# Kernel optimization log

Measured on AMD Instinct MI355X. Metric: run time of the kernel, lower is better.

The kernel has to match this reference:

```python
import jax, jax.numpy as jnp
import numpy as np

B, C, H, W = 16, 64, 128, 128
K = 3
Z = 128


def setup_inputs() -> dict:
    key = jax.random.key(0)
    k1, k2, k3, k4 = jax.random.split(key, 4)
    x = jax.random.normal(k1, (B, C, H, W), dtype=jnp.float32)
    z = jax.random.normal(k2, (B, Z), dtype=jnp.float32)
    # generator: Linear(Z -> C*C*K*K), scaled for stable conv outputs
    gen_w = jax.random.normal(k3, (Z, C * C * K * K), dtype=jnp.float32) * 0.02
    gen_b = jax.random.normal(k4, (C * C * K * K,), dtype=jnp.float32) * 0.02
    return {"x": x, "z": z, "gen_w": gen_w, "gen_b": gen_b}


def _conv_one(xi, wi):
    # xi: [C,H,W], wi: [C_out,C_in,K,K]; 'same' padding conv, no bias
    out = jax.lax.conv_general_dilated(
        xi[None], wi, window_strides=(1, 1), padding="SAME",
        dimension_numbers=("NCHW", "OIHW", "NCHW"))
    return out[0]


def reference(x, z, gen_w, gen_b):
    # per-sample weight generation: [B, C*C*K*K] -> [B, C, C, K, K]
    weight = (z @ gen_w + gen_b).reshape(B, C, C, K, K)
    # batched per-sample convolution (replaces the python loop over batch)
    return jax.vmap(_conv_one)(x, weight)
```

## Files before the change

kernel.cpp:

```cpp
#include <hip/hip_runtime.h>
#include <hip/hip_bf16.h>

typedef __attribute__((ext_vector_type(4))) float f32x4;
typedef __attribute__((ext_vector_type(8))) short short8;

#define B_ 16
#define C_ 64
#define H_ 128
#define W_ 128
#define Z_ 128
#define IDXN (C_*C_*9)
#define NT 18

__device__ __forceinline__ unsigned short f2bf(float f) {
  __hip_bfloat16 h = __float2bfloat16(f);
  return *reinterpret_cast<unsigned short*>(&h);
}

__global__ __launch_bounds__(256) void wgen_k(
    const float* __restrict__ z, const float* __restrict__ gw,
    const float* __restrict__ gb, unsigned short* __restrict__ wfrag) {
  __shared__ __align__(16) float zs[B_*Z_];
  int t = threadIdx.x;
#pragma unroll
  for (int i = 0; i < 8; ++i) zs[i*256 + t] = z[i*256 + t];
  __syncthreads();
  int lane = t & 63, bg = t >> 6;
  int b0 = bg*4;
  int idx0 = blockIdx.x*128 + lane;
  float acc[4][2];
  float bv0 = gb[idx0], bv1 = gb[idx0 + 64];
#pragma unroll
  for (int bi = 0; bi < 4; ++bi) { acc[bi][0] = bv0; acc[bi][1] = bv1; }

  for (int z0 = 0; z0 < Z_; z0 += 4) {
    float ga[4], gbv[4];
#pragma unroll
    for (int zi = 0; zi < 4; ++zi) {
      ga[zi]  = gw[(size_t)(z0+zi)*IDXN + idx0];
      gbv[zi] = gw[(size_t)(z0+zi)*IDXN + idx0 + 64];
    }
#pragma unroll
    for (int bi = 0; bi < 4; ++bi) {
      f32x4 zq = *reinterpret_cast<const f32x4*>(&zs[(b0+bi)*Z_ + z0]);
      acc[bi][0] = fmaf(zq[0], ga[0], fmaf(zq[1], ga[1], fmaf(zq[2], ga[2], fmaf(zq[3], ga[3], acc[bi][0]))));
      acc[bi][1] = fmaf(zq[0], gbv[0], fmaf(zq[1], gbv[1], fmaf(zq[2], gbv[2], fmaf(zq[3], gbv[3], acc[bi][1]))));
    }
  }
#pragma unroll
  for (int ni = 0; ni < 2; ++ni) {
    int idx = idx0 + ni*64;
    int kw = idx % 3, r1 = idx/3;
    int kh = r1 % 3, r2 = r1/3;
    int ci = r2 & 63, co = r2 >> 6;
    int k = (kh*3 + kw)*C_ + ci;
    int ts = k >> 5, kin = k & 31;
    int lm = (co & 15) | ((kin >> 3) << 4);
    int j = kin & 7, m = co >> 4;
    int base = ((ts*4 + m)*64 + lm)*8 + j;
#pragma unroll
    for (int bi = 0; bi < 4; ++bi)
      wfrag[(size_t)(b0+bi)*(NT*4*64*8) + base] = f2bf(acc[bi][ni]);
  }
}

__global__ __launch_bounds__(256) void conv_k(
    const float* __restrict__ x,
    const unsigned short* __restrict__ wfrag,
    float* __restrict__ out) {
  __shared__ __align__(16) unsigned char xs[4*130*128];
  int orig = blockIdx.x;
  int blk = (orig & 7)*128 + (orig >> 3);
  int b = blk >> 6;
  int h0 = (blk & 63)*2;
  int tid = threadIdx.x;
  int v = tid >> 6, lane = tid & 63;

  {
    int hh = h0 - 1 + v;
    bool hv = (hh >= 0) & (hh < H_);
    unsigned char* ldsrow = xs + v*(130*128);
    if (hv) {
      if (lane < 16) {
        int s = (lane < 8) ? lane : (1024 + lane - 8 + 8);
        uint4 zv; zv.x = 0; zv.y = 0; zv.z = 0; zv.w = 0;
        *reinterpret_cast<uint4*>(ldsrow + s*16) = zv;
      }
      const float* xrow = x + (((size_t)b*C_)*H_ + hh)*W_;
      int w0 = 2*lane, col0 = w0 + 1, col1 = w0 + 2;
      int g = lane >> 3;
#pragma unroll
      for (int c8 = 0; c8 < 8; ++c8) {
        int chunk = (c8 + g) & 7;
        float2 v2[8];
#pragma unroll
        for (int j = 0; j < 8; ++j)
          v2[j] = *reinterpret_cast<const float2*>(xrow + (size_t)(chunk*8 + j)*(H_*W_) + w0);
        uint4 o0, o1;
        unsigned short* s0 = reinterpret_cast<unsigned short*>(&o0);
        unsigned short* s1 = reinterpret_cast<unsigned short*>(&o1);
#pragma unroll
        for (int j = 0; j < 8; ++j) {
          s0[j] = f2bf(v2[j].x);
          s1[j] = f2bf(v2[j].y);
        }
        int a0 = col0*128 + (((chunk ^ col0) & 7) << 4);
        int a1 = col1*128 + (((chunk ^ col1) & 7) << 4);
        *reinterpret_cast<uint4*>(ldsrow + a0) = o0;
        *reinterpret_cast<uint4*>(ldsrow + a1) = o1;
      }
    } else {
      uint4 zv; zv.x = 0; zv.y = 0; zv.z = 0; zv.w = 0;
#pragma unroll
      for (int it = 0; it < 17; ++it) {
        int di = it*64 + lane;
        if (di < 1040) *reinterpret_cast<uint4*>(ldsrow + di*16) = zv;
      }
    }
  }
  __syncthreads();

  int l15 = lane & 15, lhi = lane >> 4;
  int phr = v >> 1, pw0 = (v & 1)*64;
  f32x4 acc[4][4];
#pragma unroll
  for (int mp = 0; mp < 4; ++mp)
#pragma unroll
    for (int nc = 0; nc < 4; ++nc)
      acc[mp][nc] = (f32x4){0.f, 0.f, 0.f, 0.f};

  const unsigned short* wb = wfrag + (size_t)b*(NT*4*64*8);
#pragma unroll
  for (int t = 0; t < NT; ++t) {
    int kk = t >> 1, kh = kk/3, kw = kk%3, half = t & 1;
    short8 wf[4];
#pragma unroll
    for (int nc = 0; nc < 4; ++nc)
      wf[nc] = *reinterpret_cast<const short8*>(wb + ((t*4 + nc)*64 + lane)*8);
    int chunk = half*4 + lhi;
    short8 xa[4];
#pragma unroll
    for (int mp = 0; mp < 4; ++mp) {
      int col = pw0 + mp*16 + l15 + kw;
      int addr = ((phr + kh)*130 + col)*128 + (((chunk ^ col) & 7) << 4);
      xa[mp] = *reinterpret_cast<const short8*>(&xs[addr]);
    }
#pragma unroll
    for (int mp = 0; mp < 4; ++mp)
#pragma unroll
      for (int nc = 0; nc < 4; ++nc)
        acc[mp][nc] = __builtin_amdgcn_mfma_f32_16x16x32_bf16(xa[mp], wf[nc], acc[mp][nc], 0, 0, 0);
  }

  int ph = h0 + phr;
#pragma unroll
  for (int nc = 0; nc < 4; ++nc) {
    int co = nc*16 + l15;
    float* op = out + (((size_t)b*C_ + co)*H_ + ph)*W_;
#pragma unroll
    for (int mp = 0; mp < 4; ++mp) {
      int pix = pw0 + mp*16 + lhi*4;
      *reinterpret_cast<f32x4*>(op + pix) = acc[mp][nc];
    }
  }
}

__global__ void sentinel_k(float* out, int n) {
  int i = blockIdx.x*256 + threadIdx.x;
  if (i < n) out[i] = 1.0e6f;
}

extern "C" void kernel_launch(void* const* d_in, const int* in_sizes, int n_in,
                              void* d_out, int out_size, void* d_ws, size_t ws_size,
                              hipStream_t stream) {
  const float* x  = (const float*)d_in[0];
  const float* z  = (const float*)d_in[1];
  const float* gw = (const float*)d_in[2];
  const float* gb = (const float*)d_in[3];
  float* out = (float*)d_out;

  size_t wfrag_elems = (size_t)B_*IDXN;
  size_t need = wfrag_elems*sizeof(unsigned short);
  if (ws_size < need) {
    sentinel_k<<<(out_size + 255)/256, 256, 0, stream>>>(out, out_size);
    return;
  }
  unsigned short* wfrag = (unsigned short*)d_ws;

  wgen_k <<<IDXN/128, 256, 0, stream>>>(z, gw, gb, wfrag);
  conv_k <<<B_*(H_/2),256, 0, stream>>>(x, wfrag, out);
}
```

Measured before the change: 50.45 us.

## Split conv block into 512 threads with halved per-wave output channels

Raises the conv kernel block from 256 to 512 threads, so each wave computes two output-channel tiles instead of four. This halves accumulator registers and raises occupancy. The input row staging is split across twice as many waves, each loading half the channel chunks. Weight fragments are now software-prefetched one tap ahead, and the first fragments are issued before the barrier to hide global latency. In exchange, each wave re-reads the same LDS input fragments for fewer MFMAs, which raises LDS traffic per unit of work.

Measured after the change: 51.23 us. Within noise of the previous version (+1.5%).

```diff
diff --git a/kernel.cpp b/kernel.cpp
--- a/kernel.cpp
+++ b/kernel.cpp
@@ -64,7 +64,7 @@
   }
 }
 
-__global__ __launch_bounds__(256) void conv_k(
+__global__ __launch_bounds__(512, 4) void conv_k(
     const float* __restrict__ x,
     const unsigned short* __restrict__ wfrag,
     float* __restrict__ out) {
@@ -77,12 +77,13 @@
   int v = tid >> 6, lane = tid & 63;
 
   {
-    int hh = h0 - 1 + v;
+    int r = v >> 1, hf = v & 1;
+    int hh = h0 - 1 + r;
     bool hv = (hh >= 0) & (hh < H_);
-    unsigned char* ldsrow = xs + v*(130*128);
+    unsigned char* ldsrow = xs + r*(130*128);
     if (hv) {
-      if (lane < 16) {
-        int s = (lane < 8) ? lane : (1024 + lane - 8 + 8);
+      if (lane < 8) {
+        int s = hf ? (1032 + lane) : lane;
         uint4 zv; zv.x = 0; zv.y = 0; zv.z = 0; zv.w = 0;
         *reinterpret_cast<uint4*>(ldsrow + s*16) = zv;
       }
@@ -90,8 +91,8 @@
       int w0 = 2*lane, col0 = w0 + 1, col1 = w0 + 2;
       int g = lane >> 3;
 #pragma unroll
-      for (int c8 = 0; c8 < 8; ++c8) {
-        int chunk = (c8 + g) & 7;
+      for (int i = 0; i < 4; ++i) {
+        int chunk = (hf*4 + i + g) & 7;
         float2 v2[8];
 #pragma unroll
         for (int j = 0; j < 8; ++j)
@@ -112,31 +113,38 @@
     } else {
       uint4 zv; zv.x = 0; zv.y = 0; zv.z = 0; zv.w = 0;
 #pragma unroll
-      for (int it = 0; it < 17; ++it) {
+      for (int it = 0; it < 9; ++it) {
         int di = it*64 + lane;
-        if (di < 1040) *reinterpret_cast<uint4*>(ldsrow + di*16) = zv;
+        if (di < 520) *reinterpret_cast<uint4*>(ldsrow + (hf*520 + di)*16) = zv;
       }
     }
   }
+
+  int l15 = lane & 15, lhi = lane >> 4;
+  int phr = v >> 2, pw0 = ((v >> 1) & 1)*64;
+  int mt0 = (v & 1)*2;
+  const unsigned short* wb = wfrag + (size_t)b*(NT*4*64*8);
+
+  short8 wf0 = *reinterpret_cast<const short8*>(wb + (((0*4 + mt0 + 0)*64 + lane)*8));
+  short8 wf1 = *reinterpret_cast<const short8*>(wb + (((0*4 + mt0 + 1)*64 + lane)*8));
+
   __syncthreads();
 
-  int l15 = lane & 15, lhi = lane >> 4;
-  int phr = v >> 1, pw0 = (v & 1)*64;
-  f32x4 acc[4][4];
+  f32x4 acc[4][2];
 #pragma unroll
   for (int mp = 0; mp < 4; ++mp)
 #pragma unroll
-    for (int nc = 0; nc < 4; ++nc)
+    for (int nc = 0; nc < 2; ++nc)
       acc[mp][nc] = (f32x4){0.f, 0.f, 0.f, 0.f};
 
-  const unsigned short* wb = wfrag + (size_t)b*(NT*4*64*8);
 #pragma unroll
   for (int t = 0; t < NT; ++t) {
     int kk = t >> 1, kh = kk/3, kw = kk%3, half = t & 1;
-    short8 wf[4];
-#pragma unroll
-    for (int nc = 0; nc < 4; ++nc)
-      wf[nc] = *reinterpret_cast<const short8*>(wb + ((t*4 + nc)*64 + lane)*8);
+    short8 nf0, nf1;
+    if (t + 1 < NT) {
+      nf0 = *reinterpret_cast<const short8*>(wb + ((((t+1)*4 + mt0 + 0)*64 + lane)*8));
+      nf1 = *reinterpret_cast<const short8*>(wb + ((((t+1)*4 + mt0 + 1)*64 + lane)*8));
+    }
     int chunk = half*4 + lhi;
     short8 xa[4];
 #pragma unroll
@@ -146,16 +154,17 @@
       xa[mp] = *reinterpret_cast<const short8*>(&xs[addr]);
     }
 #pragma unroll
-    for (int mp = 0; mp < 4; ++mp)
-#pragma unroll
-      for (int nc = 0; nc < 4; ++nc)
-        acc[mp][nc] = __builtin_amdgcn_mfma_f32_16x16x32_bf16(xa[mp], wf[nc], acc[mp][nc], 0, 0, 0);
+    for (int mp = 0; mp < 4; ++mp) {
+      acc[mp][0] = __builtin_amdgcn_mfma_f32_16x16x32_bf16(xa[mp], wf0, acc[mp][0], 0, 0, 0);
+      acc[mp][1] = __builtin_amdgcn_mfma_f32_16x16x32_bf16(xa[mp], wf1, acc[mp][1], 0, 0, 0);
+    }
+    wf0 = nf0; wf1 = nf1;
   }
 
   int ph = h0 + phr;
 #pragma unroll
-  for (int nc = 0; nc < 4; ++nc) {
-    int co = nc*16 + l15;
+  for (int nc = 0; nc < 2; ++nc) {
+    int co = (mt0 + nc)*16 + l15;
     float* op = out + (((size_t)b*C_ + co)*H_ + ph)*W_;
 #pragma unroll
     for (int mp = 0; mp < 4; ++mp) {
@@ -188,5 +197,5 @@
   unsigned short* wfrag = (unsigned short*)d_ws;
 
   wgen_k <<<IDXN/128, 256, 0, stream>>>(z, gw, gb, wfrag);
-  conv_k <<<B_*(H_/2),256, 0, stream>>>(x, wfrag, out);
-}
+  conv_k <<<B_*(H_/2), 512, 0, stream>>>(x, wfrag, out);
+}
```

## Enlarge conv tile to four output rows and double-buffer MFMA operand loads

Applied to the files above, without the earlier changes.

Each conv block now handles four output rows with 512 threads, staging six input rows into LDS instead of four rows for two outputs. This reduces redundant halo reads of x from global memory. The inner loop also prefetches the next tap's weight and LDS fragments while the current MFMAs run. In exchange, LDS use per block rises to about 100KB, which lowers resident blocks per CU, and two waves sit idle during staging.

After: 52.43 us. 1.04x slower.

```diff
diff --git a/kernel.cpp b/kernel.cpp
--- a/kernel.cpp
+++ b/kernel.cpp
@@ -9,6 +9,7 @@
 #define H_ 128
 #define W_ 128
 #define Z_ 128
+#define HW_ (H_*W_)
 #define IDXN (C_*C_*9)
 #define NT 18
 
@@ -64,46 +65,45 @@
   }
 }
 
-__global__ __launch_bounds__(256) void conv_k(
+__global__ __launch_bounds__(512, 2) void conv_k(
     const float* __restrict__ x,
     const unsigned short* __restrict__ wfrag,
     float* __restrict__ out) {
-  __shared__ __align__(16) unsigned char xs[4*130*128];
+  __shared__ __align__(16) unsigned char xs[6*130*128];
   int orig = blockIdx.x;
-  int blk = (orig & 7)*128 + (orig >> 3);
-  int b = blk >> 6;
-  int h0 = (blk & 63)*2;
+  int blk = (orig & 7)*64 + (orig >> 3);
+  int b = blk >> 5;
+  int h0 = (blk & 31)*4;
   int tid = threadIdx.x;
   int v = tid >> 6, lane = tid & 63;
 
-  {
+  if (tid < 96) {
+    int sl = tid >> 4, cc = (tid >> 3) & 1, ch = tid & 7;
+    int col = cc ? 129 : 0;
+    uint4 zv; zv.x = 0; zv.y = 0; zv.z = 0; zv.w = 0;
+    *reinterpret_cast<uint4*>(&xs[(sl*130 + col)*128 + ch*16]) = zv;
+  }
+
+  if (v < 6) {
     int hh = h0 - 1 + v;
     bool hv = (hh >= 0) & (hh < H_);
     unsigned char* ldsrow = xs + v*(130*128);
     if (hv) {
-      if (lane < 16) {
-        int s = (lane < 8) ? lane : (1024 + lane - 8 + 8);
-        uint4 zv; zv.x = 0; zv.y = 0; zv.z = 0; zv.w = 0;
-        *reinterpret_cast<uint4*>(ldsrow + s*16) = zv;
-      }
       const float* xrow = x + (((size_t)b*C_)*H_ + hh)*W_;
       int w0 = 2*lane, col0 = w0 + 1, col1 = w0 + 2;
       int g = lane >> 3;
 #pragma unroll
-      for (int c8 = 0; c8 < 8; ++c8) {
-        int chunk = (c8 + g) & 7;
+      for (int i = 0; i < 8; ++i) {
+        int chunk = (i + g) & 7;
         float2 v2[8];
 #pragma unroll
         for (int j = 0; j < 8; ++j)
-          v2[j] = *reinterpret_cast<const float2*>(xrow + (size_t)(chunk*8 + j)*(H_*W_) + w0);
+          v2[j] = *reinterpret_cast<const float2*>(xrow + (size_t)(chunk*8 + j)*HW_ + w0);
         uint4 o0, o1;
         unsigned short* s0 = reinterpret_cast<unsigned short*>(&o0);
         unsigned short* s1 = reinterpret_cast<unsigned short*>(&o1);
 #pragma unroll
-        for (int j = 0; j < 8; ++j) {
-          s0[j] = f2bf(v2[j].x);
-          s1[j] = f2bf(v2[j].y);
-        }
+        for (int j = 0; j < 8; ++j) { s0[j] = f2bf(v2[j].x); s1[j] = f2bf(v2[j].y); }
         int a0 = col0*128 + (((chunk ^ col0) & 7) << 4);
         int a1 = col1*128 + (((chunk ^ col1) & 7) << 4);
         *reinterpret_cast<uint4*>(ldsrow + a0) = o0;
@@ -121,7 +121,9 @@
   __syncthreads();
 
   int l15 = lane & 15, lhi = lane >> 4;
-  int phr = v >> 1, pw0 = (v & 1)*64;
+  int orow = v >> 1, pw0 = (v & 1)*64;
+  const unsigned short* wb = wfrag + (size_t)b*(NT*4*64*8);
+
   f32x4 acc[4][4];
 #pragma unroll
   for (int mp = 0; mp < 4; ++mp)
@@ -129,30 +131,46 @@
     for (int nc = 0; nc < 4; ++nc)
       acc[mp][nc] = (f32x4){0.f, 0.f, 0.f, 0.f};
 
-  const unsigned short* wb = wfrag + (size_t)b*(NT*4*64*8);
+  short8 xa0[4], xa1[4], wf0[4], wf1[4];
+  {
+    int chunk = lhi;
+    int rbase = orow*130;
+#pragma unroll
+    for (int mp = 0; mp < 4; ++mp) {
+      int col = pw0 + mp*16 + l15;
+      xa0[mp] = *reinterpret_cast<const short8*>(&xs[(rbase + col)*128 + (((chunk ^ col) & 7) << 4)]);
+    }
+#pragma unroll
+    for (int nc = 0; nc < 4; ++nc)
+      wf0[nc] = *reinterpret_cast<const short8*>(wb + ((size_t)(nc*64 + lane))*8);
+  }
+
 #pragma unroll
   for (int t = 0; t < NT; ++t) {
-    int kk = t >> 1, kh = kk/3, kw = kk%3, half = t & 1;
-    short8 wf[4];
-#pragma unroll
-    for (int nc = 0; nc < 4; ++nc)
-      wf[nc] = *reinterpret_cast<const short8*>(wb + ((t*4 + nc)*64 + lane)*8);
-    int chunk = half*4 + lhi;
-    short8 xa[4];
-#pragma unroll
-    for (int mp = 0; mp < 4; ++mp) {
-      int col = pw0 + mp*16 + l15 + kw;
-      int addr = ((phr + kh)*130 + col)*128 + (((chunk ^ col) & 7) << 4);
-      xa[mp] = *reinterpret_cast<const short8*>(&xs[addr]);
+    if (t + 1 < NT) {
+      int t1 = t + 1;
+      int kk = t1 >> 1, kh = kk/3, kw = kk - 3*kh, half = t1 & 1;
+      int chunk = half*4 + lhi;
+      int rbase = (orow + kh)*130;
+#pragma unroll
+      for (int nc = 0; nc < 4; ++nc)
+        wf1[nc] = *reinterpret_cast<const short8*>(wb + ((size_t)((t1*4 + nc)*64 + lane))*8);
+#pragma unroll
+      for (int mp = 0; mp < 4; ++mp) {
+        int col = pw0 + mp*16 + l15 + kw;
+        xa1[mp] = *reinterpret_cast<const short8*>(&xs[(rbase + col)*128 + (((chunk ^ col) & 7) << 4)]);
+      }
     }
 #pragma unroll
     for (int mp = 0; mp < 4; ++mp)
 #pragma unroll
       for (int nc = 0; nc < 4; ++nc)
-        acc[mp][nc] = __builtin_amdgcn_mfma_f32_16x16x32_bf16(xa[mp], wf[nc], acc[mp][nc], 0, 0, 0);
-  }
-
-  int ph = h0 + phr;
+        acc[mp][nc] = __builtin_amdgcn_mfma_f32_16x16x32_bf16(xa0[mp], wf0[nc], acc[mp][nc], 0, 0, 0);
+#pragma unroll
+    for (int q = 0; q < 4; ++q) { xa0[q] = xa1[q]; wf0[q] = wf1[q]; }
+  }
+
+  int ph = h0 + orow;
 #pragma unroll
   for (int nc = 0; nc < 4; ++nc) {
     int co = nc*16 + l15;
@@ -188,5 +206,5 @@
   unsigned short* wfrag = (unsigned short*)d_ws;
 
   wgen_k <<<IDXN/128, 256, 0, stream>>>(z, gw, gb, wfrag);
-  conv_k <<<B_*(H_/2),256, 0, stream>>>(x, wfrag, out);
-}
+  conv_k <<<B_*(H_/4), 512, 0, stream>>>(x, wfrag, out);
+}
```
